# Optimization experiments

Hardware: AMD Instinct MI355X
Metric: run time of the kernel (lower is better)

The kernel has to match this reference:

```python
import jax, jax.numpy as jnp
import numpy as np

B, L = 2048, 4096


def setup_inputs() -> dict:
    key = jax.random.key(0)
    k1, k2, k3 = jax.random.split(key, 3)
    j = jax.random.normal(k1, (1,), dtype=jnp.float32)
    b = jax.random.normal(k2, (2,), dtype=jnp.float32)
    observations = jax.random.randint(k3, (B, L), 0, 2, dtype=jnp.int64)
    return {"j": j, "b": b, "observations": observations}


def reference(j, b, observations):
    dt = j.dtype
    values = jnp.array([-0.5, 0.5], dtype=dt)           # 2 latent states
    pairs = values[:, None] * values[None, :]            # [2,2] outer product
    psi = j * pairs                                      # pairwise max-plus potential [2,2]
    # unary potentials: phi[b_idx, i, s] = b[obs[b_idx, i]] * values[s]
    phi = b[observations][..., None] * values            # [B, L, 2]
    zeros2 = jnp.zeros((2,), dtype=dt)

    def step(msg, phi_i):
        # max-plus message update: max over source state s of phi[s] + psi[s,t] + msg[s]
        new = jnp.max(phi_i[:, None] + psi + msg[:, None], axis=0)
        return new, new

    def per_seq(phi_seq):  # phi_seq: [L, 2]
        # forward messages: column 0 is zeros, column i+1 is msg from step i (i = 0..L-2)
        _, f = jax.lax.scan(step, zeros2, phi_seq[:-1])
        fwd = jnp.concatenate([zeros2[None], f], axis=0)       # [L, 2]
        # backward messages: iterate i = L-1 down to 1; msg from step i lands at column i-1
        _, bk = jax.lax.scan(step, zeros2, phi_seq[:0:-1])
        bwd = jnp.concatenate([bk[::-1], zeros2[None]], axis=0)  # [L, 2]
        return (phi_seq + fwd + bwd).T                          # [2, L]

    return jax.vmap(per_seq)(phi)  # [B, 2, L]
```

## Files before the change

kernel.cpp:

```cpp
#include <hip/hip_runtime.h>
#include <math.h>

#define L_SEQ 4096
#define NT 512
#define CHUNK 8
#define NW (NT/64)

struct M2 { float a00, a01, a10, a11; };

__device__ __forceinline__ M2 mpc(const M2& A, const M2& B) {
  M2 C;
  C.a00 = fmaxf(A.a00 + B.a00, A.a01 + B.a10);
  C.a01 = fmaxf(A.a00 + B.a01, A.a01 + B.a11);
  C.a10 = fmaxf(A.a10 + B.a00, A.a11 + B.a10);
  C.a11 = fmaxf(A.a10 + B.a01, A.a11 + B.a11);
  return C;
}

__global__ __launch_bounds__(NT, 8) void chain_fb_kernel(
    const float* __restrict__ jp, const float* __restrict__ bp,
    const int* __restrict__ obs, float* __restrict__ out) {
  __shared__ float4 wtf[NW];
  __shared__ float4 wtb[NW];

  const int t = threadIdx.x;
  const int lane = t & 63;
  const int w = t >> 6;
  const long b = blockIdx.x;

  const float P   = 0.25f * jp[0];
  const float hb0 = 0.5f * bp[0];
  const float hb1 = 0.5f * bp[1];

  const int4* rowp = (const int4*)(obs + b * L_SEQ + (long)t * CHUNK);
  int4 q0 = rowp[0], q1 = rowp[1];
  int ov[CHUNK] = {q0.x, q0.y, q0.z, q0.w, q1.x, q1.y, q1.z, q1.w};
  float u[CHUNK];
  #pragma unroll
  for (int e = 0; e < CHUNK; ++e) u[e] = ov[e] ? hb1 : hb0;

  M2 T{P - u[0], -u[0] - P, u[0] - P, u[0] + P};
  #pragma unroll
  for (int e = 1; e < CHUNK; ++e) {
    float x0 = T.a00 - u[e], y0 = T.a01 + u[e];
    float x1 = T.a10 - u[e], y1 = T.a11 + u[e];
    T.a00 = fmaxf(x0 + P, y0 - P); T.a01 = fmaxf(x0 - P, y0 + P);
    T.a10 = fmaxf(x1 + P, y1 - P); T.a11 = fmaxf(x1 - P, y1 + P);
  }
  M2 R{P - u[CHUNK-1], -u[CHUNK-1] - P, u[CHUNK-1] - P, u[CHUNK-1] + P};
  #pragma unroll
  for (int e = CHUNK - 2; e >= 0; --e) {
    float x0 = R.a00 - u[e], y0 = R.a01 + u[e];
    float x1 = R.a10 - u[e], y1 = R.a11 + u[e];
    R.a00 = fmaxf(x0 + P, y0 - P); R.a01 = fmaxf(x0 - P, y0 + P);
    R.a10 = fmaxf(x1 + P, y1 - P); R.a11 = fmaxf(x1 - P, y1 + P);
  }

  #pragma unroll
  for (int off = 1; off < 64; off <<= 1) {
    M2 OF{__shfl_up(T.a00, off), __shfl_up(T.a01, off),
          __shfl_up(T.a10, off), __shfl_up(T.a11, off)};
    M2 OB{__shfl_down(R.a00, off), __shfl_down(R.a01, off),
          __shfl_down(R.a10, off), __shfl_down(R.a11, off)};
    if (lane >= off)      T = mpc(OF, T);
    if (lane < 64 - off)  R = mpc(OB, R);
  }
  if (lane == 63) wtf[w] = make_float4(T.a00, T.a01, T.a10, T.a11);
  if (lane == 0)  wtb[w] = make_float4(R.a00, R.a01, R.a10, R.a11);

  M2 EF{__shfl_up(T.a00, 1), __shfl_up(T.a01, 1),
        __shfl_up(T.a10, 1), __shfl_up(T.a11, 1)};
  M2 EB{__shfl_down(R.a00, 1), __shfl_down(R.a01, 1),
        __shfl_down(R.a10, 1), __shfl_down(R.a11, 1)};
  if (lane == 0)  { EF.a00 = 0.f; EF.a01 = -INFINITY; EF.a10 = -INFINITY; EF.a11 = 0.f; }
  if (lane == 63) { EB.a00 = 0.f; EB.a01 = -INFINITY; EB.a10 = -INFINITY; EB.a11 = 0.f; }

  __syncthreads();

  M2 GF = EF, GB = EB;
  for (int ww = w - 1; ww >= 0; --ww) {
    float4 a = wtf[ww];
    GF = mpc(M2{a.x, a.y, a.z, a.w}, GF);
  }
  for (int ww = w + 1; ww < NW; ++ww) {
    float4 a = wtb[ww];
    GB = mpc(M2{a.x, a.y, a.z, a.w}, GB);
  }
  float fm0 = fmaxf(GF.a00, GF.a10), fm1 = fmaxf(GF.a01, GF.a11);
  float bm0 = fmaxf(GB.a00, GB.a10), bm1 = fmaxf(GB.a01, GB.a11);

  float o0[CHUNK], o1[CHUNK];
  #pragma unroll
  for (int e = 0; e < CHUNK; ++e) {
    float x = fm0 - u[e], y = fm1 + u[e];
    o0[e] = x; o1[e] = y;
    fm0 = fmaxf(x + P, y - P);
    fm1 = fmaxf(x - P, y + P);
  }
  #pragma unroll
  for (int e = CHUNK - 1; e >= 0; --e) {
    o0[e] += bm0; o1[e] += bm1;
    float x = bm0 - u[e], y = bm1 + u[e];
    bm0 = fmaxf(x + P, y - P);
    bm1 = fmaxf(x - P, y + P);
  }

  const long base = (long)t * CHUNK;
  float* r0 = out + b * (2L * L_SEQ) + base;
  float* r1 = r0 + L_SEQ;
  ((float4*)r0)[0] = make_float4(o0[0], o0[1], o0[2], o0[3]);
  ((float4*)r0)[1] = make_float4(o0[4], o0[5], o0[6], o0[7]);
  ((float4*)r1)[0] = make_float4(o1[0], o1[1], o1[2], o1[3]);
  ((float4*)r1)[1] = make_float4(o1[4], o1[5], o1[6], o1[7]);
}

extern "C" void kernel_launch(void* const* d_in, const int* in_sizes, int n_in,
                              void* d_out, int out_size, void* d_ws, size_t ws_size,
                              hipStream_t stream) {
  const float* jp  = (const float*)d_in[0];
  const float* bp  = (const float*)d_in[1];
  const int*   obs = (const int*)d_in[2];
  float* out = (float*)d_out;
  const int B = in_sizes[2] / L_SEQ;
  chain_fb_kernel<<<B, NT, 0, stream>>>(jp, bp, obs, out);
}
```

Baseline: 25.72 us.

## Replace per-chunk transfer-matrix products with shared-memory lookup tables over bit patterns

Each thread packs its 16 binary observations into a bitmask. The block then builds a table of the 16 possible 4-step max-plus transfer matrices, combines pairs of them into a 256-entry table of 8-step matrices in LDS, and forms the 16-step forward and reversed products with a single max-plus multiply of two lookups. This removes most of the per-thread serial chunk-reduction arithmetic. The block size is halved and the chunk length doubled, which adds two extra barriers and leaves fewer threads in flight per block.

```diff
diff --git a/kernel.cpp b/kernel.cpp
--- a/kernel.cpp
+++ b/kernel.cpp
@@ -2,8 +2,8 @@
 #include <math.h>
 
 #define L_SEQ 4096
-#define NT 512
-#define CHUNK 8
+#define NT 256
+#define CHUNK 16
 #define NW (NT/64)
 
 struct M2 { float a00, a01, a10, a11; };
@@ -17,9 +17,14 @@
   return C;
 }
 
-__global__ __launch_bounds__(NT, 8) void chain_fb_kernel(
+__device__ __forceinline__ M2 ldm(const float4& v) { return M2{v.x, v.y, v.z, v.w}; }
+__device__ __forceinline__ float4 stm(const M2& m) { return make_float4(m.a00, m.a01, m.a10, m.a11); }
+
+__global__ __launch_bounds__(NT, 4) void chain_fb_kernel(
     const float* __restrict__ jp, const float* __restrict__ bp,
     const int* __restrict__ obs, float* __restrict__ out) {
+  __shared__ float4 T4s[16];
+  __shared__ float4 T8s[256];
   __shared__ float4 wtf[NW];
   __shared__ float4 wtb[NW];
 
@@ -33,28 +38,31 @@
   const float hb1 = 0.5f * bp[1];
 
   const int4* rowp = (const int4*)(obs + b * L_SEQ + (long)t * CHUNK);
-  int4 q0 = rowp[0], q1 = rowp[1];
-  int ov[CHUNK] = {q0.x, q0.y, q0.z, q0.w, q1.x, q1.y, q1.z, q1.w};
-  float u[CHUNK];
+  int4 q0 = rowp[0], q1 = rowp[1], q2 = rowp[2], q3 = rowp[3];
+  int ov[CHUNK] = {q0.x, q0.y, q0.z, q0.w, q1.x, q1.y, q1.z, q1.w,
+                   q2.x, q2.y, q2.z, q2.w, q3.x, q3.y, q3.z, q3.w};
+  unsigned m = 0;
   #pragma unroll
-  for (int e = 0; e < CHUNK; ++e) u[e] = ov[e] ? hb1 : hb0;
+  for (int e = 0; e < CHUNK; ++e) m |= (unsigned)(ov[e] & 1) << e;
 
-  M2 T{P - u[0], -u[0] - P, u[0] - P, u[0] + P};
-  #pragma unroll
-  for (int e = 1; e < CHUNK; ++e) {
-    float x0 = T.a00 - u[e], y0 = T.a01 + u[e];
-    float x1 = T.a10 - u[e], y1 = T.a11 + u[e];
-    T.a00 = fmaxf(x0 + P, y0 - P); T.a01 = fmaxf(x0 - P, y0 + P);
-    T.a10 = fmaxf(x1 + P, y1 - P); T.a11 = fmaxf(x1 - P, y1 + P);
+  if (t < 16) {
+    float u0 = (t & 1) ? hb1 : hb0;
+    M2 Tt{P - u0, -u0 - P, u0 - P, u0 + P};
+    #pragma unroll
+    for (int k = 1; k < 4; ++k) {
+      float uk = ((t >> k) & 1) ? hb1 : hb0;
+      M2 Ek{P - uk, -uk - P, uk - P, uk + P};
+      Tt = mpc(Tt, Ek);
+    }
+    T4s[t] = stm(Tt);
   }
-  M2 R{P - u[CHUNK-1], -u[CHUNK-1] - P, u[CHUNK-1] - P, u[CHUNK-1] + P};
-  #pragma unroll
-  for (int e = CHUNK - 2; e >= 0; --e) {
-    float x0 = R.a00 - u[e], y0 = R.a01 + u[e];
-    float x1 = R.a10 - u[e], y1 = R.a11 + u[e];
-    R.a00 = fmaxf(x0 + P, y0 - P); R.a01 = fmaxf(x0 - P, y0 + P);
-    R.a10 = fmaxf(x1 + P, y1 - P); R.a11 = fmaxf(x1 - P, y1 + P);
-  }
+  __syncthreads();
+  T8s[t] = stm(mpc(ldm(T4s[t & 15]), ldm(T4s[(t >> 4) & 15])));
+  __syncthreads();
+
+  unsigned r16 = __brev(m) >> 16;
+  M2 T = mpc(ldm(T8s[m & 255]),   ldm(T8s[(m >> 8) & 255]));
+  M2 R = mpc(ldm(T8s[r16 & 255]), ldm(T8s[(r16 >> 8) & 255]));
 
   #pragma unroll
   for (int off = 1; off < 64; off <<= 1) {
@@ -65,8 +73,8 @@
     if (lane >= off)      T = mpc(OF, T);
     if (lane < 64 - off)  R = mpc(OB, R);
   }
-  if (lane == 63) wtf[w] = make_float4(T.a00, T.a01, T.a10, T.a11);
-  if (lane == 0)  wtb[w] = make_float4(R.a00, R.a01, R.a10, R.a11);
+  if (lane == 63) wtf[w] = stm(T);
+  if (lane == 0)  wtb[w] = stm(R);
 
   M2 EF{__shfl_up(T.a00, 1), __shfl_up(T.a01, 1),
         __shfl_up(T.a10, 1), __shfl_up(T.a11, 1)};
@@ -78,29 +86,25 @@
   __syncthreads();
 
   M2 GF = EF, GB = EB;
-  for (int ww = w - 1; ww >= 0; --ww) {
-    float4 a = wtf[ww];
-    GF = mpc(M2{a.x, a.y, a.z, a.w}, GF);
-  }
-  for (int ww = w + 1; ww < NW; ++ww) {
-    float4 a = wtb[ww];
-    GB = mpc(M2{a.x, a.y, a.z, a.w}, GB);
-  }
+  for (int ww = w - 1; ww >= 0; --ww) GF = mpc(ldm(wtf[ww]), GF);
+  for (int ww = w + 1; ww < NW; ++ww) GB = mpc(ldm(wtb[ww]), GB);
   float fm0 = fmaxf(GF.a00, GF.a10), fm1 = fmaxf(GF.a01, GF.a11);
   float bm0 = fmaxf(GB.a00, GB.a10), bm1 = fmaxf(GB.a01, GB.a11);
 
   float o0[CHUNK], o1[CHUNK];
   #pragma unroll
   for (int e = 0; e < CHUNK; ++e) {
-    float x = fm0 - u[e], y = fm1 + u[e];
+    float u = ((m >> e) & 1) ? hb1 : hb0;
+    float x = fm0 - u, y = fm1 + u;
     o0[e] = x; o1[e] = y;
     fm0 = fmaxf(x + P, y - P);
     fm1 = fmaxf(x - P, y + P);
   }
   #pragma unroll
   for (int e = CHUNK - 1; e >= 0; --e) {
+    float u = ((m >> e) & 1) ? hb1 : hb0;
     o0[e] += bm0; o1[e] += bm1;
-    float x = bm0 - u[e], y = bm1 + u[e];
+    float x = bm0 - u, y = bm1 + u;
     bm0 = fmaxf(x + P, y - P);
     bm1 = fmaxf(x - P, y + P);
   }
@@ -108,10 +112,11 @@
   const long base = (long)t * CHUNK;
   float* r0 = out + b * (2L * L_SEQ) + base;
   float* r1 = r0 + L_SEQ;
-  ((float4*)r0)[0] = make_float4(o0[0], o0[1], o0[2], o0[3]);
-  ((float4*)r0)[1] = make_float4(o0[4], o0[5], o0[6], o0[7]);
-  ((float4*)r1)[0] = make_float4(o1[0], o1[1], o1[2], o1[3]);
-  ((float4*)r1)[1] = make_float4(o1[4], o1[5], o1[6], o1[7]);
+  #pragma unroll
+  for (int v = 0; v < CHUNK / 4; ++v) {
+    ((float4*)r0)[v] = make_float4(o0[4*v], o0[4*v+1], o0[4*v+2], o0[4*v+3]);
+    ((float4*)r1)[v] = make_float4(o1[4*v], o1[4*v+1], o1[4*v+2], o1[4*v+3]);
+  }
 }
 
 extern "C" void kernel_launch(void* const* d_in, const int* in_sizes, int n_in,
```

Measured after the change: 32.64 us. +26.9%, slower.
